# Kernel tuning notes

Hardware: AMD Instinct MI355X
Metric: run time of the kernel (lower is better)

## Reference

```python
import jax, jax.numpy as jnp
import numpy as np

N, E, H, IN, C, L, G = 50000, 600000, 128, 128, 4, 3, 128
EPS = 1e-5
BN_SCALE = 1.0 / np.sqrt(1.0 + EPS)  # eval BN with running_mean=0, running_var=1


def _bn(x, g, b):
    return x * (g * BN_SCALE) + b


def _gelu(x):
    return jax.nn.gelu(x, approximate=False)


def setup_inputs() -> dict:
    key = jax.random.key(0)
    ks = jax.random.split(key, 40)
    s = 0.02
    d = {}
    d['x'] = jax.random.normal(ks[0], (N, IN), jnp.float32)
    d['edge_index'] = jax.random.randint(ks[1], (2, E), 0, N)
    d['batch'] = jnp.sort(jax.random.randint(ks[2], (N,), 0, G))
    # input projection
    d['W1'] = jax.random.normal(ks[3], (IN, H)) * s; d['b1'] = jnp.zeros((H,))
    d['g1'] = jnp.ones((H,)); d['be1'] = jnp.zeros((H,))
    d['W2'] = jax.random.normal(ks[4], (H, H)) * s; d['b2'] = jnp.zeros((H,))
    d['g2'] = jnp.ones((H,)); d['be2'] = jnp.zeros((H,))
    # GCN layers (stacked over L)
    d['Wg'] = jax.random.normal(ks[5], (L, H, H)) * s
    d['bg'] = jnp.zeros((L, H))
    d['gg'] = jnp.ones((L, H)); d['bgg'] = jnp.zeros((L, H))
    # graph attention weights
    d['Wa1'] = jax.random.normal(ks[6], (H, H // 2)) * s; d['ba1'] = jnp.zeros((H // 2,))
    d['Wa2'] = jax.random.normal(ks[7], (H // 2, 1)) * s; d['ba2'] = jnp.zeros((1,))
    # classifier
    d['Wc1'] = jax.random.normal(ks[8], (4 * H, 2 * H)) * s; d['bc1'] = jnp.zeros((2 * H,))
    d['gc1'] = jnp.ones((2 * H,)); d['bec1'] = jnp.zeros((2 * H,))
    d['Wc2'] = jax.random.normal(ks[9], (2 * H, H)) * s; d['bc2'] = jnp.zeros((H,))
    d['gc2'] = jnp.ones((H,)); d['bec2'] = jnp.zeros((H,))
    d['Wc3'] = jax.random.normal(ks[10], (H, H // 2)) * s; d['bc3'] = jnp.zeros((H // 2,))
    d['gc3'] = jnp.ones((H // 2,)); d['bec3'] = jnp.zeros((H // 2,))
    d['Wc4'] = jax.random.normal(ks[11], (H // 2, C)) * s; d['bc4'] = jnp.zeros((C,))
    return d


def reference(x, edge_index, batch, W1, b1, g1, be1, W2, b2, g2, be2,
              Wg, bg, gg, bgg, Wa1, ba1, Wa2, ba2,
              Wc1, bc1, gc1, bec1, Wc2, bc2, gc2, bec2,
              Wc3, bc3, gc3, bec3, Wc4, bc4):
    n = x.shape[0]
    src, dst = edge_index[0], edge_index[1]
    # input projection (dropout off in eval)
    h = _gelu(_bn(x @ W1 + b1, g1, be1))
    h = _gelu(_bn(h @ W2 + b2, g2, be2))
    # GCN symmetric norm with self-loops (PyG GCNConv semantics)
    deg = jax.ops.segment_sum(jnp.ones_like(src, dtype=h.dtype), dst, n) + 1.0
    dinv = jax.lax.rsqrt(deg)
    enorm = (dinv[src] * dinv[dst])[:, None]   # [E,1]
    snorm = (dinv * dinv)[:, None]             # [N,1] self-loop weight
    for i in range(L):
        xw = h @ Wg[i]
        agg = jax.ops.segment_sum(xw[src] * enorm, dst, n) + xw * snorm
        h = _gelu(_bn(agg + bg[i], gg[i], bgg[i])) + h
    # attention weights per node
    aw = jnp.tanh(_gelu(h @ Wa1 + ba1) @ Wa2 + ba2)  # [N,1]
    # multi-branch pooling per graph
    cnt = jnp.maximum(jax.ops.segment_sum(jnp.ones((n,), h.dtype), batch, G), 1.0)[:, None]
    x_mean = jax.ops.segment_sum(h, batch, G) / cnt
    x_max = jax.ops.segment_max(h, batch, G)
    x_weighted = jax.ops.segment_sum(h * aw, batch, G) / cnt
    comb = jnp.concatenate([x_mean, x_max, x_mean, x_weighted], axis=-1)  # x_transformer_pooled == x_mean
    z = _gelu(_bn(comb @ Wc1 + bc1, gc1, bec1))
    z = _gelu(_bn(z @ Wc2 + bc2, gc2, bec2))
    z = _gelu(_bn(z @ Wc3 + bc3, gc3, bec3))
    return z @ Wc4 + bc4
```

## Files before the change

kernel.cpp:

```cpp
#include <hip/hip_runtime.h>
#include <hip/hip_bf16.h>
#include <float.h>


#define GGRAPHS 128
#define POOL_NC 16

typedef __attribute__((ext_vector_type(8))) short short8b;
typedef __attribute__((ext_vector_type(4))) float f32x4;

__device__ __forceinline__ float gelu_f(float x) {
    return 0.5f * x * (1.0f + erff(x * 0.7071067811865476f));
}

__device__ __forceinline__ unsigned short f2bf(float f) {
    unsigned int u = __float_as_uint(f);
    unsigned int r = (u + 0x7FFFu + ((u >> 16) & 1u)) >> 16;
    return (unsigned short)r;
}

__device__ __forceinline__ float bf2f(unsigned short u) {
    return __uint_as_float(((unsigned int)u) << 16);
}

static constexpr float BNS_F = 0.99999500003749968f;

__global__ void tobf_kernel(const float4* __restrict__ X, ushort4* __restrict__ Xb, int n4)
{
    int id = blockIdx.x * 256 + threadIdx.x;
    if (id < n4) {
        float4 v = X[id];
        ushort4 q;
        q.x = f2bf(v.x); q.y = f2bf(v.y); q.z = f2bf(v.z); q.w = f2bf(v.w);
        Xb[id] = q;
    }
}

__global__ void transpose_bf_kernel(const float* __restrict__ W, unsigned short* __restrict__ Wt,
                                    int K, int M)
{
    int id = blockIdx.x * 256 + threadIdx.x;
    if (id < K * M) {
        int k = id / M, c = id % M;
        Wt[c * K + k] = f2bf(W[id]);
    }
}

template<int M, bool DO_BN, bool DO_GELU, bool DO_RES, bool DO_AW, bool DO_F32, bool DO_BF16>
__global__ __launch_bounds__(256, 2)
void gemm_mfma(const unsigned short* __restrict__ Abf,
               const unsigned short* __restrict__ Wtb,
               const float* __restrict__ bias, const float* __restrict__ gam,
               const float* __restrict__ beta, const float* __restrict__ resid,
               float* __restrict__ Yf, unsigned short* __restrict__ Ybf,
               const float* __restrict__ Wa2, const float* __restrict__ ba2,
               float* __restrict__ awout, int nrows)
{
    constexpr int NCT = M / 16;
    __shared__ unsigned short Wl[M * 128];

    const int tid = threadIdx.x;

    constexpr int NCH = M * 16;
#pragma unroll
    for (int i = 0; i < NCH / 256; ++i) {
        const int idx = i * 256 + tid;
        const uint4 v = reinterpret_cast<const uint4*>(Wtb)[idx];
        const int byte = idx * 16;
        const int swz = byte ^ (((byte >> 8) & 7) << 4);
        *reinterpret_cast<uint4*>(reinterpret_cast<char*>(Wl) + swz) = v;
    }
    __syncthreads();

    const int w = tid >> 6;
    const int l = tid & 63;
    const int l4 = l >> 4, lm = l & 15;
    const int rowbase = (int)blockIdx.x * 64 + w * 16;

    int arow = rowbase + lm; if (arow >= nrows) arow = nrows - 1;
    const unsigned short* ap = Abf + (size_t)arow * 128 + l4 * 8;
    short8b a[4];
#pragma unroll
    for (int ks = 0; ks < 4; ++ks)
        a[ks] = *reinterpret_cast<const short8b*>(ap + ks * 32);

    f32x4 acc[NCT];
#pragma unroll
    for (int ct = 0; ct < NCT; ++ct) acc[ct] = f32x4{0.f, 0.f, 0.f, 0.f};

    const int swzm = (lm & 7) << 4;
    const char* Wlc = reinterpret_cast<const char*>(Wl);
#pragma unroll
    for (int ks = 0; ks < 4; ++ks) {
#pragma unroll
        for (int ct = 0; ct < NCT; ++ct) {
            const int byte = ct * 4096 + lm * 256 + ks * 64 + l4 * 16;
            const short8b bv = *reinterpret_cast<const short8b*>(Wlc + (byte ^ swzm));
            acc[ct] = __builtin_amdgcn_mfma_f32_16x16x32_bf16(a[ks], bv, acc[ct], 0, 0, 0);
        }
    }

    if (DO_AW) {
        float p[4] = {0.f, 0.f, 0.f, 0.f};
#pragma unroll
        for (int ct = 0; ct < NCT; ++ct) {
            const int col = ct * 16 + lm;
            float sc, bi;
            if (DO_BN) { float g = gam[col]; sc = g * BNS_F; bi = bias[col] * sc + beta[col]; }
            else       { sc = 1.f; bi = bias[col]; }
            const float wa = Wa2[col];
#pragma unroll
            for (int rid = 0; rid < 4; ++rid) {
                float v = acc[ct][rid] * sc + bi;
                if (DO_GELU) v = gelu_f(v);
                p[rid] = fmaf(v, wa, p[rid]);
            }
        }
        const float ba2v = ba2[0];
#pragma unroll
        for (int rid = 0; rid < 4; ++rid) {
            float v = p[rid];
            v += __shfl_xor(v, 1);
            v += __shfl_xor(v, 2);
            v += __shfl_xor(v, 4);
            v += __shfl_xor(v, 8);
            const int row = rowbase + l4 * 4 + rid;
            if (lm == 0 && row < nrows) awout[row] = tanhf(v + ba2v);
        }
        return;
    }

#pragma unroll
    for (int ct = 0; ct < NCT; ++ct) {
        const int col = ct * 16 + lm;
        float sc, bi;
        if (DO_BN) { float g = gam[col]; sc = g * BNS_F; bi = bias[col] * sc + beta[col]; }
        else       { sc = 1.f; bi = bias[col]; }
#pragma unroll
        for (int rid = 0; rid < 4; ++rid) {
            const int row = rowbase + l4 * 4 + rid;
            if (row < nrows) {
                float v = acc[ct][rid] * sc + bi;
                if (DO_GELU) v = gelu_f(v);
                if (DO_RES) v += resid[(size_t)row * M + col];
                if (DO_F32) Yf[(size_t)row * M + col] = v;
                if (DO_BF16) Ybf[(size_t)row * M + col] = f2bf(v);
            }
        }
    }
}

__global__ void count_rank_kernel(const int* __restrict__ dst, int* __restrict__ cnt,
                                  int* __restrict__ rank, int E)
{
    int e = blockIdx.x * 256 + threadIdx.x;
    if (e < E) rank[e] = atomicAdd(&cnt[dst[e]], 1);
}

__global__ void scan_local(const int* __restrict__ cnt, int* __restrict__ rowptr,
                           int* __restrict__ bsum, float* __restrict__ dinv, int n)
{
    __shared__ int sd[1024];
    const int tid = threadIdx.x;
    const int i = blockIdx.x * 1024 + tid;
    int v = (i < n) ? cnt[i] : 0;
    if (i < n) dinv[i] = rsqrtf((float)v + 1.0f);
    sd[tid] = v;
    __syncthreads();
    for (int off = 1; off < 1024; off <<= 1) {
        int t = (tid >= off) ? sd[tid - off] : 0;
        __syncthreads();
        sd[tid] += t;
        __syncthreads();
    }
    if (i < n) rowptr[i + 1] = sd[tid];
    if (tid == 1023) bsum[blockIdx.x] = sd[1023];
}

__global__ void scan_bsum(int* __restrict__ bsum, int nb)
{
    const int lane = threadIdx.x;
    int orig = (lane < nb) ? bsum[lane] : 0;
    int v = orig;
#pragma unroll
    for (int off = 1; off < 64; off <<= 1) {
        int t = __shfl_up(v, off);
        if (lane >= off) v += t;
    }
    if (lane < nb) bsum[lane] = v - orig;
}

__global__ void scan_add(int* __restrict__ rowptr, const int* __restrict__ bsum, int n)
{
    const int i = blockIdx.x * 1024 + threadIdx.x;
    if (i < n) rowptr[i + 1] += bsum[blockIdx.x];
    if (i == 0) rowptr[0] = 0;
}

__global__ void fill_kernel(const int* __restrict__ src, const int* __restrict__ dst,
                            const float* __restrict__ dinv, const int* __restrict__ rowptr,
                            const int* __restrict__ rank, int2* __restrict__ csr, int E)
{
    int e = blockIdx.x * 256 + threadIdx.x;
    if (e < E) {
        const int d = dst[e], s = src[e];
        const int pos = rowptr[d] + rank[e];
        int2 p;
        p.x = s;
        p.y = __float_as_int(dinv[s] * dinv[d]);
        csr[pos] = p;
    }
}

#define FMAB(A, Wt, U) { A.x = fmaf(Wt, bf2f(U.x), A.x); A.y = fmaf(Wt, bf2f(U.y), A.y); \
                         A.z = fmaf(Wt, bf2f(U.z), A.z); A.w = fmaf(Wt, bf2f(U.w), A.w); }

__global__ __launch_bounds__(256)
void agg_kernel(const ushort4* __restrict__ hb, const int2* __restrict__ csr,
                const int* __restrict__ rowptr, const float* __restrict__ dinv,
                ushort4* __restrict__ ahb, int n)
{
    const int node = blockIdx.x * 8 + (threadIdx.x >> 5);
    if (node >= n) return;
    const int lane = threadIdx.x & 31;

    const float di = dinv[node];
    const float sw = di * di;
    const ushort4 sv = hb[(size_t)node * 32 + lane];
    float4 a0, a1;
    a0.x = bf2f(sv.x) * sw; a0.y = bf2f(sv.y) * sw;
    a0.z = bf2f(sv.z) * sw; a0.w = bf2f(sv.w) * sw;
    a1.x = 0.f; a1.y = 0.f; a1.z = 0.f; a1.w = 0.f;

    const int beg = rowptr[node], end = rowptr[node + 1];
    int s = beg;
    for (; s + 4 <= end; s += 4) {
        const int2 e0 = csr[s+0], e1 = csr[s+1], e2 = csr[s+2], e3 = csr[s+3];
        const ushort4 v0 = hb[(size_t)e0.x * 32 + lane];
        const ushort4 v1 = hb[(size_t)e1.x * 32 + lane];
        const ushort4 v2 = hb[(size_t)e2.x * 32 + lane];
        const ushort4 v3 = hb[(size_t)e3.x * 32 + lane];
        FMAB(a0, __int_as_float(e0.y), v0); FMAB(a1, __int_as_float(e1.y), v1);
        FMAB(a0, __int_as_float(e2.y), v2); FMAB(a1, __int_as_float(e3.y), v3);
    }
    for (; s < end; ++s) {
        const int2 e0 = csr[s];
        const ushort4 v = hb[(size_t)e0.x * 32 + lane];
        FMAB(a0, __int_as_float(e0.y), v);
    }
    ushort4 q;
    q.x = f2bf(a0.x + a1.x); q.y = f2bf(a0.y + a1.y);
    q.z = f2bf(a0.z + a1.z); q.w = f2bf(a0.w + a1.w);
    ahb[(size_t)node * 32 + lane] = q;
}

__global__ void bounds_kernel(const int* __restrict__ batch, int* __restrict__ bound, int n, int g)
{
    const int t = blockIdx.x * blockDim.x + threadIdx.x;
    if (t > g) return;
    int lo = 0, hi = n;
    while (lo < hi) { int mid = (lo + hi) >> 1; if (batch[mid] < t) lo = mid + 1; else hi = mid; }
    bound[t] = lo;
}

__global__ void pool_partial(const float* __restrict__ h, const float* __restrict__ aw,
                             const int* __restrict__ bound, float* __restrict__ ps,
                             float* __restrict__ pm, float* __restrict__ pw)
{
    const int g = blockIdx.x >> 4;
    const int c = blockIdx.x & (POOL_NC - 1);
    const int f = threadIdx.x;
    const int beg = bound[g], end = bound[g + 1];
    const int len = end - beg;
    const int cbeg = beg + (int)(((long long)len * c) / POOL_NC);
    const int cend = beg + (int)(((long long)len * (c + 1)) / POOL_NC);
    float s = 0.f, m = -FLT_MAX, w = 0.f;
    for (int node = cbeg; node < cend; ++node) {
        const float v = h[(size_t)node * 128 + f];
        const float a = aw[node];
        s += v;
        m = fmaxf(m, v);
        w = fmaf(v, a, w);
    }
    const size_t idx = ((size_t)g * POOL_NC + c) * 128 + f;
    ps[idx] = s; pm[idx] = m; pw[idx] = w;
}

__global__ void pool_final(const float* __restrict__ ps, const float* __restrict__ pm,
                           const float* __restrict__ pw, const int* __restrict__ bound,
                           float* __restrict__ comb)
{
    const int g = blockIdx.x;
    const int f = threadIdx.x;
    float s = 0.f, m = -FLT_MAX, w = 0.f;
#pragma unroll
    for (int c = 0; c < POOL_NC; ++c) {
        const size_t idx = ((size_t)g * POOL_NC + c) * 128 + f;
        s += ps[idx];
        m = fmaxf(m, pm[idx]);
        w += pw[idx];
    }
    float cn = (float)(bound[g + 1] - bound[g]);
    if (cn < 1.f) cn = 1.f;
    comb[(size_t)g * 512 + f]       = s / cn;
    comb[(size_t)g * 512 + 128 + f] = m;
    comb[(size_t)g * 512 + 256 + f] = s / cn;
    comb[(size_t)g * 512 + 384 + f] = w / cn;
}

template<int K, int M, bool DO_BN, bool DO_GELU>
__global__ __launch_bounds__(256)
void rowgemm2(const float* __restrict__ X, const float* __restrict__ W,
              const float* __restrict__ bias, const float* __restrict__ gam,
              const float* __restrict__ beta, float* __restrict__ Y)
{
    constexpr int NC = M / 64;
    constexpr int KQ = K / 4;
    const int row = blockIdx.x / NC;
    const int lane = threadIdx.x & 63;
    const int c = (blockIdx.x % NC) * 64 + lane;
    const int q = threadIdx.x >> 6;

    const float* __restrict__ xq = X + (size_t)row * K + q * KQ;
    const float* __restrict__ wq = W + (size_t)(q * KQ) * M + c;

    float a0 = 0.f, a1 = 0.f, a2 = 0.f, a3 = 0.f;
#pragma unroll 4
    for (int k = 0; k < KQ; k += 4) {
        const float4 xv = *reinterpret_cast<const float4*>(xq + k);
        a0 = fmaf(xv.x, wq[(size_t)(k + 0) * M], a0);
        a1 = fmaf(xv.y, wq[(size_t)(k + 1) * M], a1);
        a2 = fmaf(xv.z, wq[(size_t)(k + 2) * M], a2);
        a3 = fmaf(xv.w, wq[(size_t)(k + 3) * M], a3);
    }
    __shared__ float part[4][64];
    part[q][lane] = (a0 + a1) + (a2 + a3);
    __syncthreads();
    if (q == 0) {
        float v = (part[0][lane] + part[1][lane]) + (part[2][lane] + part[3][lane]);
        if (DO_BN) { const float g = gam[c]; const float sc = g * BNS_F; v = v * sc + (bias[c] * sc + beta[c]); }
        else       { v = v + bias[c]; }
        if (DO_GELU) v = gelu_f(v);
        Y[(size_t)row * M + c] = v;
    }
}

__global__ void rowgemm_final(const float* __restrict__ X, const float* __restrict__ W,
                              const float* __restrict__ bias, float* __restrict__ Y)
{
    const int row = blockIdx.x;
    const int lane = threadIdx.x;
    const float xv = X[(size_t)row * 64 + lane];
    const float4 wr = *reinterpret_cast<const float4*>(W + lane * 4);
    float a0 = xv * wr.x, a1 = xv * wr.y, a2 = xv * wr.z, a3 = xv * wr.w;
#pragma unroll
    for (int off = 32; off; off >>= 1) {
        a0 += __shfl_xor(a0, off);
        a1 += __shfl_xor(a1, off);
        a2 += __shfl_xor(a2, off);
        a3 += __shfl_xor(a3, off);
    }
    if (lane == 0) {
        Y[(size_t)row * 4 + 0] = a0 + bias[0];
        Y[(size_t)row * 4 + 1] = a1 + bias[1];
        Y[(size_t)row * 4 + 2] = a2 + bias[2];
        Y[(size_t)row * 4 + 3] = a3 + bias[3];
    }
}

extern "C" void kernel_launch(void* const* d_in, const int* in_sizes, int n_in,
                              void* d_out, int out_size, void* d_ws, size_t ws_size,
                              hipStream_t stream)
{
    const float* x     = (const float*)d_in[0];
    const int*   ei    = (const int*)d_in[1];
    const int*   batch = (const int*)d_in[2];
    const float* W1  = (const float*)d_in[3];
    const float* b1  = (const float*)d_in[4];
    const float* g1  = (const float*)d_in[5];
    const float* be1 = (const float*)d_in[6];
    const float* W2  = (const float*)d_in[7];
    const float* b2  = (const float*)d_in[8];
    const float* g2  = (const float*)d_in[9];
    const float* be2 = (const float*)d_in[10];
    const float* Wg  = (const float*)d_in[11];
    const float* bg  = (const float*)d_in[12];
    const float* gg  = (const float*)d_in[13];
    const float* bgg = (const float*)d_in[14];
    const float* Wa1 = (const float*)d_in[15];
    const float* ba1 = (const float*)d_in[16];
    const float* Wa2 = (const float*)d_in[17];
    const float* ba2 = (const float*)d_in[18];
    const float* Wc1 = (const float*)d_in[19];
    const float* bc1 = (const float*)d_in[20];
    const float* gc1 = (const float*)d_in[21];
    const float* bec1= (const float*)d_in[22];
    const float* Wc2 = (const float*)d_in[23];
    const float* bc2 = (const float*)d_in[24];
    const float* gc2 = (const float*)d_in[25];
    const float* bec2= (const float*)d_in[26];
    const float* Wc3 = (const float*)d_in[27];
    const float* bc3 = (const float*)d_in[28];
    const float* gc3 = (const float*)d_in[29];
    const float* bec3= (const float*)d_in[30];
    const float* Wc4 = (const float*)d_in[31];
    const float* bc4 = (const float*)d_in[32];
    float* out = (float*)d_out;

    const int N = in_sizes[0] / 128;
    const int E = in_sizes[1] / 2;
    const int G = GGRAPHS;

    size_t off = 0;
    auto alloc = [&](size_t bytes) -> void* {
        void* p = (char*)d_ws + off;
        off += (bytes + 255) & ~(size_t)255;
        return p;
    };
    float*          hB    = (float*)alloc((size_t)N * 128 * 4);
    unsigned short* xb    = (unsigned short*)alloc((size_t)N * 128 * 2);
    unsigned short* hAb   = (unsigned short*)alloc((size_t)N * 128 * 2);
    unsigned short* hbf   = (unsigned short*)alloc((size_t)N * 128 * 2);
    unsigned short* ahb   = (unsigned short*)alloc((size_t)N * 128 * 2);
    unsigned short* Wt1   = (unsigned short*)alloc(128 * 128 * 2);
    unsigned short* Wt2   = (unsigned short*)alloc(128 * 128 * 2);
    unsigned short* Wtg   = (unsigned short*)alloc(3 * 128 * 128 * 2);
    unsigned short* Wta1  = (unsigned short*)alloc(64 * 128 * 2);
    float*   aw     = (float*)alloc((size_t)N * 4);
    float*   dinv   = (float*)alloc((size_t)N * 4);
    int*     cnt    = (int*)alloc((size_t)N * 4);
    int*     rank   = (int*)alloc((size_t)E * 4);
    int*     rowptr = (int*)alloc((size_t)(N + 1) * 4);
    int*     bsum   = (int*)alloc(64 * 4);
    int2*    csr    = (int2*)alloc((size_t)E * 8);
    int*     bound  = (int*)alloc((size_t)(G + 1) * 4);
    float*   comb   = (float*)alloc((size_t)G * 512 * 4);
    float*   ps     = (float*)alloc((size_t)G * POOL_NC * 128 * 4);
    float*   pm     = (float*)alloc((size_t)G * POOL_NC * 128 * 4);
    float*   pw     = (float*)alloc((size_t)G * POOL_NC * 128 * 4);
    float*   z1     = (float*)alloc((size_t)G * 256 * 4);
    float*   z2     = (float*)alloc((size_t)G * 128 * 4);
    float*   z3     = (float*)alloc((size_t)G * 64 * 4);
    (void)ws_size;

    const int* e_src = ei;
    const int* e_dst = ei + E;

    tobf_kernel<<<(N * 32 + 255) / 256, 256, 0, stream>>>(
        (const float4*)x, (ushort4*)xb, N * 32);
    transpose_bf_kernel<<<64, 256, 0, stream>>>(W1, Wt1, 128, 128);
    transpose_bf_kernel<<<64, 256, 0, stream>>>(W2, Wt2, 128, 128);
    for (int l = 0; l < 3; ++l)
        transpose_bf_kernel<<<64, 256, 0, stream>>>(Wg + (size_t)l * 16384, Wtg + (size_t)l * 16384, 128, 128);
    transpose_bf_kernel<<<32, 256, 0, stream>>>(Wa1, Wta1, 128, 64);

    hipMemsetAsync(cnt, 0, (size_t)N * 4, stream);
    count_rank_kernel<<<(E + 255) / 256, 256, 0, stream>>>(e_dst, cnt, rank, E);
    const int nb = (N + 1023) / 1024;
    scan_local<<<nb, 1024, 0, stream>>>(cnt, rowptr, bsum, dinv, N);
    scan_bsum<<<1, 64, 0, stream>>>(bsum, nb);
    scan_add<<<nb, 1024, 0, stream>>>(rowptr, bsum, N);
    fill_kernel<<<(E + 255) / 256, 256, 0, stream>>>(e_src, e_dst, dinv, rowptr, rank, csr, E);

    const int rowblocks = (N + 63) / 64;

    gemm_mfma<128, true, true, false, false, false, true><<<rowblocks, 256, 0, stream>>>(
        xb, Wt1, b1, g1, be1, nullptr, nullptr, hAb, nullptr, nullptr, nullptr, N);
    gemm_mfma<128, true, true, false, false, true, true><<<rowblocks, 256, 0, stream>>>(
        hAb, Wt2, b2, g2, be2, nullptr, hB, hbf, nullptr, nullptr, nullptr, N);

    for (int l = 0; l < 3; ++l) {
        agg_kernel<<<(N + 7) / 8, 256, 0, stream>>>(
            (const ushort4*)hbf, csr, rowptr, dinv, (ushort4*)ahb, N);
        gemm_mfma<128, true, true, true, false, true, true><<<rowblocks, 256, 0, stream>>>(
            ahb, Wtg + (size_t)l * 16384, bg + (size_t)l * 128,
            gg + (size_t)l * 128, bgg + (size_t)l * 128, hB, hB, hbf,
            nullptr, nullptr, nullptr, N);
    }

    gemm_mfma<64, false, true, false, true, false, false><<<rowblocks, 256, 0, stream>>>(
        hbf, Wta1, ba1, nullptr, nullptr, nullptr, nullptr, nullptr, Wa2, ba2, aw, N);

    bounds_kernel<<<1, 256, 0, stream>>>(batch, bound, N, G);
    pool_partial<<<G * POOL_NC, 128, 0, stream>>>(hB, aw, bound, ps, pm, pw);
    pool_final<<<G, 128, 0, stream>>>(ps, pm, pw, bound, comb);

    rowgemm2<512, 256, true, true><<<G * 4, 256, 0, stream>>>(comb, Wc1, bc1, gc1, bec1, z1);
    rowgemm2<256, 128, true, true><<<G * 2, 256, 0, stream>>>(z1, Wc2, bc2, gc2, bec2, z2);
    rowgemm2<128, 64,  true, true><<<G * 1, 256, 0, stream>>>(z2, Wc3, bc3, gc3, bec3, z3);
    rowgemm_final<<<G, 64, 0, stream>>>(z3, Wc4, bc4, out);
}
```

Before: 413.9 us.

## Drop fp32 hidden state, fuse input bf16 conversion and weight transposes

Removes the fp32 copy of the hidden state: the residual is now read from the bf16 buffer and the GEMM epilogue writes only bf16, which cuts global traffic in each GCN layer and in pooling. The fp32-to-bf16 conversion of x moves into the first GEMM's A-load, and the six weight transpose launches merge into one kernel. The bounds kernel is replaced by inline binary searches in the pooling kernels. The cost is precision: the residual stream now accumulates in bf16 across layers, and the GEMM reads and writes hbf in place.

```diff
diff --git a/kernel.cpp b/kernel.cpp
--- a/kernel.cpp
+++ b/kernel.cpp
@@ -25,34 +25,33 @@
 
 static constexpr float BNS_F = 0.99999500003749968f;
 
-__global__ void tobf_kernel(const float4* __restrict__ X, ushort4* __restrict__ Xb, int n4)
-{
-    int id = blockIdx.x * 256 + threadIdx.x;
-    if (id < n4) {
-        float4 v = X[id];
-        ushort4 q;
-        q.x = f2bf(v.x); q.y = f2bf(v.y); q.z = f2bf(v.z); q.w = f2bf(v.w);
-        Xb[id] = q;
-    }
-}
-
-__global__ void transpose_bf_kernel(const float* __restrict__ W, unsigned short* __restrict__ Wt,
-                                    int K, int M)
-{
-    int id = blockIdx.x * 256 + threadIdx.x;
-    if (id < K * M) {
-        int k = id / M, c = id % M;
-        Wt[c * K + k] = f2bf(W[id]);
-    }
-}
-
-template<int M, bool DO_BN, bool DO_GELU, bool DO_RES, bool DO_AW, bool DO_F32, bool DO_BF16>
+__global__ void transpose_all_kernel(const float* __restrict__ W1, const float* __restrict__ W2,
+                                     const float* __restrict__ Wg, const float* __restrict__ Wa1,
+                                     unsigned short* __restrict__ Wt1, unsigned short* __restrict__ Wt2,
+                                     unsigned short* __restrict__ Wtg, unsigned short* __restrict__ Wta1)
+{
+    const int id = blockIdx.x * 256 + threadIdx.x;
+    if (id < 81920) {
+        const int m = id >> 14;
+        const int r = id & 16383;
+        const int k = r >> 7, c = r & 127;
+        const float* Wsrc = (m == 0) ? W1 : (m == 1) ? W2 : Wg + (size_t)(m - 2) * 16384;
+        unsigned short* Wdst = (m == 0) ? Wt1 : (m == 1) ? Wt2 : Wtg + (size_t)(m - 2) * 16384;
+        Wdst[c * 128 + k] = f2bf(Wsrc[r]);
+    } else if (id < 90112) {
+        const int r = id - 81920;
+        const int k = r >> 6, c = r & 63;
+        Wta1[c * 128 + k] = f2bf(Wa1[r]);
+    }
+}
+
+template<int M, bool A_FP32, bool DO_BN, bool DO_GELU, bool DO_RES, bool DO_AW>
 __global__ __launch_bounds__(256, 2)
-void gemm_mfma(const unsigned short* __restrict__ Abf,
+void gemm_mfma(const void* __restrict__ Ain,
                const unsigned short* __restrict__ Wtb,
                const float* __restrict__ bias, const float* __restrict__ gam,
-               const float* __restrict__ beta, const float* __restrict__ resid,
-               float* __restrict__ Yf, unsigned short* __restrict__ Ybf,
+               const float* __restrict__ beta, const unsigned short* __restrict__ residb,
+               unsigned short* __restrict__ Ybf,
                const float* __restrict__ Wa2, const float* __restrict__ ba2,
                float* __restrict__ awout, int nrows)
 {
@@ -78,11 +77,26 @@
     const int rowbase = (int)blockIdx.x * 64 + w * 16;
 
     int arow = rowbase + lm; if (arow >= nrows) arow = nrows - 1;
-    const unsigned short* ap = Abf + (size_t)arow * 128 + l4 * 8;
     short8b a[4];
-#pragma unroll
-    for (int ks = 0; ks < 4; ++ks)
-        a[ks] = *reinterpret_cast<const short8b*>(ap + ks * 32);
+    if constexpr (A_FP32) {
+        const float* apf = (const float*)Ain + (size_t)arow * 128 + l4 * 8;
+#pragma unroll
+        for (int ks = 0; ks < 4; ++ks) {
+            const float4 v0 = *reinterpret_cast<const float4*>(apf + ks * 32);
+            const float4 v1 = *reinterpret_cast<const float4*>(apf + ks * 32 + 4);
+            short8b av;
+            av[0] = (short)f2bf(v0.x); av[1] = (short)f2bf(v0.y);
+            av[2] = (short)f2bf(v0.z); av[3] = (short)f2bf(v0.w);
+            av[4] = (short)f2bf(v1.x); av[5] = (short)f2bf(v1.y);
+            av[6] = (short)f2bf(v1.z); av[7] = (short)f2bf(v1.w);
+            a[ks] = av;
+        }
+    } else {
+        const unsigned short* ap = (const unsigned short*)Ain + (size_t)arow * 128 + l4 * 8;
+#pragma unroll
+        for (int ks = 0; ks < 4; ++ks)
+            a[ks] = *reinterpret_cast<const short8b*>(ap + ks * 32);
+    }
 
     f32x4 acc[NCT];
 #pragma unroll
@@ -142,9 +156,8 @@
             if (row < nrows) {
                 float v = acc[ct][rid] * sc + bi;
                 if (DO_GELU) v = gelu_f(v);
-                if (DO_RES) v += resid[(size_t)row * M + col];
-                if (DO_F32) Yf[(size_t)row * M + col] = v;
-                if (DO_BF16) Ybf[(size_t)row * M + col] = f2bf(v);
+                if (DO_RES) v += bf2f(residb[(size_t)row * M + col]);
+                Ybf[(size_t)row * M + col] = f2bf(v);
             }
         }
     }
@@ -254,29 +267,27 @@
     ahb[(size_t)node * 32 + lane] = q;
 }
 
-__global__ void bounds_kernel(const int* __restrict__ batch, int* __restrict__ bound, int n, int g)
-{
-    const int t = blockIdx.x * blockDim.x + threadIdx.x;
-    if (t > g) return;
+__device__ __forceinline__ int lb_batch(const int* __restrict__ batch, int n, int t)
+{
     int lo = 0, hi = n;
     while (lo < hi) { int mid = (lo + hi) >> 1; if (batch[mid] < t) lo = mid + 1; else hi = mid; }
-    bound[t] = lo;
-}
-
-__global__ void pool_partial(const float* __restrict__ h, const float* __restrict__ aw,
-                             const int* __restrict__ bound, float* __restrict__ ps,
+    return lo;
+}
+
+__global__ void pool_partial(const unsigned short* __restrict__ h, const float* __restrict__ aw,
+                             const int* __restrict__ batch, int n, float* __restrict__ ps,
                              float* __restrict__ pm, float* __restrict__ pw)
 {
     const int g = blockIdx.x >> 4;
     const int c = blockIdx.x & (POOL_NC - 1);
     const int f = threadIdx.x;
-    const int beg = bound[g], end = bound[g + 1];
+    const int beg = lb_batch(batch, n, g), end = lb_batch(batch, n, g + 1);
     const int len = end - beg;
     const int cbeg = beg + (int)(((long long)len * c) / POOL_NC);
     const int cend = beg + (int)(((long long)len * (c + 1)) / POOL_NC);
     float s = 0.f, m = -FLT_MAX, w = 0.f;
     for (int node = cbeg; node < cend; ++node) {
-        const float v = h[(size_t)node * 128 + f];
+        const float v = bf2f(h[(size_t)node * 128 + f]);
         const float a = aw[node];
         s += v;
         m = fmaxf(m, v);
@@ -287,8 +298,8 @@
 }
 
 __global__ void pool_final(const float* __restrict__ ps, const float* __restrict__ pm,
-                           const float* __restrict__ pw, const int* __restrict__ bound,
-                           float* __restrict__ comb)
+                           const float* __restrict__ pw, const int* __restrict__ batch,
+                           int n, float* __restrict__ comb)
 {
     const int g = blockIdx.x;
     const int f = threadIdx.x;
@@ -300,7 +311,7 @@
         m = fmaxf(m, pm[idx]);
         w += pw[idx];
     }
-    float cn = (float)(bound[g + 1] - bound[g]);
+    float cn = (float)(lb_batch(batch, n, g + 1) - lb_batch(batch, n, g));
     if (cn < 1.f) cn = 1.f;
     comb[(size_t)g * 512 + f]       = s / cn;
     comb[(size_t)g * 512 + 128 + f] = m;
@@ -417,8 +428,6 @@
         off += (bytes + 255) & ~(size_t)255;
         return p;
     };
-    float*          hB    = (float*)alloc((size_t)N * 128 * 4);
-    unsigned short* xb    = (unsigned short*)alloc((size_t)N * 128 * 2);
     unsigned short* hAb   = (unsigned short*)alloc((size_t)N * 128 * 2);
     unsigned short* hbf   = (unsigned short*)alloc((size_t)N * 128 * 2);
     unsigned short* ahb   = (unsigned short*)alloc((size_t)N * 128 * 2);
@@ -433,7 +442,6 @@
     int*     rowptr = (int*)alloc((size_t)(N + 1) * 4);
     int*     bsum   = (int*)alloc(64 * 4);
     int2*    csr    = (int2*)alloc((size_t)E * 8);
-    int*     bound  = (int*)alloc((size_t)(G + 1) * 4);
     float*   comb   = (float*)alloc((size_t)G * 512 * 4);
     float*   ps     = (float*)alloc((size_t)G * POOL_NC * 128 * 4);
     float*   pm     = (float*)alloc((size_t)G * POOL_NC * 128 * 4);
@@ -446,13 +454,7 @@
     const int* e_src = ei;
     const int* e_dst = ei + E;
 
-    tobf_kernel<<<(N * 32 + 255) / 256, 256, 0, stream>>>(
-        (const float4*)x, (ushort4*)xb, N * 32);
-    transpose_bf_kernel<<<64, 256, 0, stream>>>(W1, Wt1, 128, 128);
-    transpose_bf_kernel<<<64, 256, 0, stream>>>(W2, Wt2, 128, 128);
-    for (int l = 0; l < 3; ++l)
-        transpose_bf_kernel<<<64, 256, 0, stream>>>(Wg + (size_t)l * 16384, Wtg + (size_t)l * 16384, 128, 128);
-    transpose_bf_kernel<<<32, 256, 0, stream>>>(Wa1, Wta1, 128, 64);
+    transpose_all_kernel<<<352, 256, 0, stream>>>(W1, W2, Wg, Wa1, Wt1, Wt2, Wtg, Wta1);
 
     hipMemsetAsync(cnt, 0, (size_t)N * 4, stream);
     count_rank_kernel<<<(E + 255) / 256, 256, 0, stream>>>(e_dst, cnt, rank, E);
@@ -464,26 +466,25 @@
 
     const int rowblocks = (N + 63) / 64;
 
-    gemm_mfma<128, true, true, false, false, false, true><<<rowblocks, 256, 0, stream>>>(
-        xb, Wt1, b1, g1, be1, nullptr, nullptr, hAb, nullptr, nullptr, nullptr, N);
-    gemm_mfma<128, true, true, false, false, true, true><<<rowblocks, 256, 0, stream>>>(
-        hAb, Wt2, b2, g2, be2, nullptr, hB, hbf, nullptr, nullptr, nullptr, N);
+    gemm_mfma<128, true, true, true, false, false><<<rowblocks, 256, 0, stream>>>(
+        x, Wt1, b1, g1, be1, nullptr, hAb, nullptr, nullptr, nullptr, N);
+    gemm_mfma<128, false, true, true, false, false><<<rowblocks, 256, 0, stream>>>(
+        hAb, Wt2, b2, g2, be2, nullptr, hbf, nullptr, nullptr, nullptr, N);
 
     for (int l = 0; l < 3; ++l) {
         agg_kernel<<<(N + 7) / 8, 256, 0, stream>>>(
             (const ushort4*)hbf, csr, rowptr, dinv, (ushort4*)ahb, N);
-        gemm_mfma<128, true, true, true, false, true, true><<<rowblocks, 256, 0, stream>>>(
+        gemm_mfma<128, false, true, true, true, false><<<rowblocks, 256, 0, stream>>>(
             ahb, Wtg + (size_t)l * 16384, bg + (size_t)l * 128,
-            gg + (size_t)l * 128, bgg + (size_t)l * 128, hB, hB, hbf,
+            gg + (size_t)l * 128, bgg + (size_t)l * 128, hbf, hbf,
             nullptr, nullptr, nullptr, N);
     }
 
-    gemm_mfma<64, false, true, false, true, false, false><<<rowblocks, 256, 0, stream>>>(
-        hbf, Wta1, ba1, nullptr, nullptr, nullptr, nullptr, nullptr, Wa2, ba2, aw, N);
-
-    bounds_kernel<<<1, 256, 0, stream>>>(batch, bound, N, G);
-    pool_partial<<<G * POOL_NC, 128, 0, stream>>>(hB, aw, bound, ps, pm, pw);
-    pool_final<<<G, 128, 0, stream>>>(ps, pm, pw, bound, comb);
+    gemm_mfma<64, false, false, true, false, true><<<rowblocks, 256, 0, stream>>>(
+        hbf, Wta1, ba1, nullptr, nullptr, nullptr, nullptr, Wa2, ba2, aw, N);
+
+    pool_partial<<<G * POOL_NC, 128, 0, stream>>>(hbf, aw, batch, N, ps, pm, pw);
+    pool_final<<<G, 128, 0, stream>>>(ps, pm, pw, batch, N, comb);
 
     rowgemm2<512, 256, true, true><<<G * 4, 256, 0, stream>>>(comb, Wc1, bc1, gc1, bec1, z1);
     rowgemm2<256, 128, true, true><<<G * 2, 256, 0, stream>>>(z1, Wc2, bc2, gc2, bec2, z2);
```

After: 382.6 us. 1.08x faster.
